# Performance work log

Hardware: AMD Instinct MI355X
Metric: run time of the kernel (lower is better)

Reference implementation:

```python
import jax, jax.numpy as jnp
import numpy as np

B, S, D = 8, 8192, 64   # D = 2**n_qubits, n_qubits = 6
D_MODEL = 1024
EPS = 1e-8


def setup_inputs() -> dict:
    key = jax.random.key(0)
    ks = jax.random.split(key, 7)
    return {
        "psi_Q": jax.random.normal(ks[0], (B, S, D), dtype=jnp.float32),
        "psi_K": jax.random.normal(ks[1], (B, S, D), dtype=jnp.float32),
        "psi_V": jax.random.normal(ks[2], (B, S, D), dtype=jnp.float32),
        "W1": jax.random.normal(ks[3], (1, D_MODEL), dtype=jnp.float32) * 0.02,
        "b1": jnp.zeros((D_MODEL,), dtype=jnp.float32),
        "W2": jax.random.normal(ks[4], (D_MODEL, D_MODEL), dtype=jnp.float32) * 0.02,
        "b2": jnp.zeros((D_MODEL,), dtype=jnp.float32),
    }


def _l2norm(x):
    return x / (jnp.linalg.norm(x, axis=-1, keepdims=True) + EPS)


def reference(psi_Q, psi_K, psi_V, W1, b1, W2, b2):
    # Normalize states (as the torch module does before StatePrep)
    q = _l2norm(psi_Q)
    k = _l2norm(psi_K)
    v = _l2norm(psi_V)
    state_dim = q.shape[-1]  # 2**n_qubits

    # attention_circuit probs[0]:
    # amplitude<0...0| = (H^{\otimes n} q)[0] * k[0] = sum(q)/sqrt(2^n) * k[0]
    att = (jnp.sum(q, axis=-1) ** 2) * (k[..., 0] ** 2) / state_dim  # [B,S]

    # value_circuit <Z_0>: wire 0 is MSB -> first half +1, second half -1
    half = state_dim // 2
    v2 = v * v
    v_exp = jnp.sum(v2[..., :half], axis=-1) - jnp.sum(v2[..., half:], axis=-1)  # [B,S]

    xi = (att * v_exp)[..., None]  # [B,S,1]

    h = jax.nn.relu(xi @ W1 + b1)   # [B,S,d_model]
    yQ = h @ W2 + b2                # [B,S,d_model]
    return yQ, xi
```

## Files before the change

### kernel.cpp

```cpp
#include <hip/hip_runtime.h>
#include <math.h>

#define BB 8
#define SS 8192
#define DD 64
#define DM 1024
#define EPSF 1e-8f
#define NROWS (BB * SS)
#define YQ_ELEMS ((size_t)NROWS * DM)

#define NPBLK 64

typedef float floatx4 __attribute__((ext_vector_type(4)));


__global__ __launch_bounds__(256) void qac_prep(
    const float* __restrict__ psiQ, const float* __restrict__ psiK,
    const float* __restrict__ psiV, const float* __restrict__ W1,
    const float* __restrict__ b1, const float* __restrict__ W2,
    const float* __restrict__ b2, float* __restrict__ ws,
    float* __restrict__ out) {
  const int t = threadIdx.x;

  if (blockIdx.x < NPBLK) {
    __shared__ float red[4][16][16];
    const int tn = t & 15;
    const int tm = t >> 4;
    const int nb = blockIdx.x;
    const int n = nb * 16 + tn;

    float up = 0.f, un = 0.f, dp = 0.f, dn = 0.f;
    const int m0 = tm * 64;
#pragma unroll 8
    for (int i = 0; i < 64; ++i) {
      const int m = m0 + i;
      const float w1 = W1[m];
      const float bv = b1[m];
      const float w2 = W2[(size_t)m * DM + n];
      const float wp = w1 > 0.f ? w1 : 0.f;
      const float wn = w1 < 0.f ? w1 : 0.f;
      const float bp = w1 > 0.f ? bv : 0.f;
      const float bn = w1 < 0.f ? bv : 0.f;
      up = fmaf(wp, w2, up);
      un = fmaf(wn, w2, un);
      dp = fmaf(bp, w2, dp);
      dn = fmaf(bn, w2, dn);
    }
    red[0][tm][tn] = up;
    red[1][tm][tn] = un;
    red[2][tm][tn] = dp;
    red[3][tm][tn] = dn;
    __syncthreads();
    if (t < 64) {
      const int q = t >> 4;
      const int col = t & 15;
      float s = 0.f;
#pragma unroll
      for (int j = 0; j < 16; ++j) s += red[q][j][col];
      const int n2 = nb * 16 + col;
      if (q < 2) {
        ws[q * DM + n2] = s;
      } else {
        ws[q * DM + n2] = b2[n2] + s;
      }
    }
    return;
  }

  const int g = t & 15;
  const int grp = t >> 4;
  const int row = (blockIdx.x - NPBLK) * 16 + grp;

  const float4 q = ((const float4*)(psiQ + (size_t)row * DD))[g];
  const float4 k = ((const float4*)(psiK + (size_t)row * DD))[g];
  const float4 v = ((const float4*)(psiV + (size_t)row * DD))[g];

  float sq = q.x + q.y + q.z + q.w;
  float sq2 = q.x * q.x + q.y * q.y + q.z * q.z + q.w * q.w;
  float sk2 = k.x * k.x + k.y * k.y + k.z * k.z + k.w * k.w;
  const float v2 = v.x * v.x + v.y * v.y + v.z * v.z + v.w * v.w;
  float va = (g < 8) ? v2 : 0.f;
  float vb = (g < 8) ? 0.f : v2;
  const float k0 = k.x;

#pragma unroll
  for (int m = 1; m < 16; m <<= 1) {
    sq += __shfl_xor(sq, m);
    sq2 += __shfl_xor(sq2, m);
    sk2 += __shfl_xor(sk2, m);
    va += __shfl_xor(va, m);
    vb += __shfl_xor(vb, m);
  }
  if (g == 0) {
    const float nq = sqrtf(sq2) + EPSF;
    const float nk = sqrtf(sk2) + EPSF;
    const float nv = sqrtf(va + vb) + EPSF;
    const float sqn = sq / nq;
    const float k0n = k0 / nk;
    const float att = sqn * sqn * k0n * k0n * (1.0f / 64.0f);
    const float vexp = (va - vb) / (nv * nv);
    out[YQ_ELEMS + row] = att * vexp;
  }
}

__global__ __launch_bounds__(256) void qac_stream(
    const float* __restrict__ ws, float* __restrict__ out) {
  __shared__ float xis[64];
  const int t = threadIdx.x;
  const int r0 = blockIdx.x * 64;
  if (t < 64) xis[t] = out[YQ_ELEMS + r0 + t];

  const float4 up = ((const float4*)(ws))[t];
  const float4 un = ((const float4*)(ws + DM))[t];
  const float4 cp = ((const float4*)(ws + 2 * DM))[t];
  const float4 cn = ((const float4*)(ws + 3 * DM))[t];
  __syncthreads();

#pragma unroll 8
  for (int r = 0; r < 64; ++r) {
    const float xi = xis[r];
    const bool pos = xi > 0.f;
    floatx4 o;
    o.x = fmaf(xi, pos ? up.x : un.x, pos ? cp.x : cn.x);
    o.y = fmaf(xi, pos ? up.y : un.y, pos ? cp.y : cn.y);
    o.z = fmaf(xi, pos ? up.z : un.z, pos ? cp.z : cn.z);
    o.w = fmaf(xi, pos ? up.w : un.w, pos ? cp.w : cn.w);
    floatx4* dst = (floatx4*)(out + (size_t)(r0 + r) * DM) + t;
    __builtin_nontemporal_store(o, dst);
  }
}

extern "C" void kernel_launch(void* const* d_in, const int* in_sizes, int n_in,
                              void* d_out, int out_size, void* d_ws, size_t ws_size,
                              hipStream_t stream) {
  const float* psiQ = (const float*)d_in[0];
  const float* psiK = (const float*)d_in[1];
  const float* psiV = (const float*)d_in[2];
  const float* W1 = (const float*)d_in[3];
  const float* b1 = (const float*)d_in[4];
  const float* W2 = (const float*)d_in[5];
  const float* b2 = (const float*)d_in[6];
  float* out = (float*)d_out;
  float* ws = (float*)d_ws;

  qac_prep<<<NPBLK + NROWS / 16, 256, 0, stream>>>(psiQ, psiK, psiV, W1, b1,
                                                   W2, b2, ws, out);
  qac_stream<<<NROWS / 64, 256, 0, stream>>>(ws, out);
}
```

Before: 63.98 us.

## Fuse per-row xi computation into the output streaming kernel

Splits the W1/W2 precompute into its own small kernel and moves the per-row quantum-state reductions into the streaming kernel, so each block computes its 64 xi values in shared memory before writing the output rows. This removes the global write and re-read of xi between kernels, and the first kernel is now tiny, so most of the work sits in a single pass. Input loads now use nontemporal hints. The risk is that the fused kernel's longer prologue delays the start of its store stream and may reduce overlap.

Measured after the change: 66.90 us. 1.05x slower.

```diff
diff --git a/kernel.cpp b/kernel.cpp
--- a/kernel.cpp
+++ b/kernel.cpp
@@ -9,112 +9,112 @@
 #define NROWS (BB * SS)
 #define YQ_ELEMS ((size_t)NROWS * DM)
 
-#define NPBLK 64
-
 typedef float floatx4 __attribute__((ext_vector_type(4)));
 
 
-__global__ __launch_bounds__(256) void qac_prep(
-    const float* __restrict__ psiQ, const float* __restrict__ psiK,
-    const float* __restrict__ psiV, const float* __restrict__ W1,
-    const float* __restrict__ b1, const float* __restrict__ W2,
-    const float* __restrict__ b2, float* __restrict__ ws,
-    float* __restrict__ out) {
+__global__ __launch_bounds__(256) void qac_part(
+    const float* __restrict__ W1, const float* __restrict__ b1,
+    const float* __restrict__ W2, const float* __restrict__ b2,
+    float* __restrict__ ws) {
+  __shared__ float red[4][16][16];
   const int t = threadIdx.x;
+  const int tn = t & 15;
+  const int tm = t >> 4;
+  const int nb = blockIdx.x;
+  const int n = nb * 16 + tn;
 
-  if (blockIdx.x < NPBLK) {
-    __shared__ float red[4][16][16];
-    const int tn = t & 15;
-    const int tm = t >> 4;
-    const int nb = blockIdx.x;
-    const int n = nb * 16 + tn;
-
-    float up = 0.f, un = 0.f, dp = 0.f, dn = 0.f;
-    const int m0 = tm * 64;
+  float up = 0.f, un = 0.f, dp = 0.f, dn = 0.f;
+  const int m0 = tm * 64;
 #pragma unroll 8
-    for (int i = 0; i < 64; ++i) {
-      const int m = m0 + i;
-      const float w1 = W1[m];
-      const float bv = b1[m];
-      const float w2 = W2[(size_t)m * DM + n];
-      const float wp = w1 > 0.f ? w1 : 0.f;
-      const float wn = w1 < 0.f ? w1 : 0.f;
-      const float bp = w1 > 0.f ? bv : 0.f;
-      const float bn = w1 < 0.f ? bv : 0.f;
-      up = fmaf(wp, w2, up);
-      un = fmaf(wn, w2, un);
-      dp = fmaf(bp, w2, dp);
-      dn = fmaf(bn, w2, dn);
+  for (int i = 0; i < 64; ++i) {
+    const int m = m0 + i;
+    const float w1 = W1[m];
+    const float bv = b1[m];
+    const float w2 = W2[(size_t)m * DM + n];
+    const float wp = w1 > 0.f ? w1 : 0.f;
+    const float wn = w1 < 0.f ? w1 : 0.f;
+    const float bp = w1 > 0.f ? bv : 0.f;
+    const float bn = w1 < 0.f ? bv : 0.f;
+    up = fmaf(wp, w2, up);
+    un = fmaf(wn, w2, un);
+    dp = fmaf(bp, w2, dp);
+    dn = fmaf(bn, w2, dn);
+  }
+  red[0][tm][tn] = up;
+  red[1][tm][tn] = un;
+  red[2][tm][tn] = dp;
+  red[3][tm][tn] = dn;
+  __syncthreads();
+  if (t < 64) {
+    const int q = t >> 4;
+    const int col = t & 15;
+    float s = 0.f;
+#pragma unroll
+    for (int j = 0; j < 16; ++j) s += red[q][j][col];
+    const int n2 = nb * 16 + col;
+    if (q < 2) {
+      ws[q * DM + n2] = s;
+    } else {
+      ws[q * DM + n2] = b2[n2] + s;
     }
-    red[0][tm][tn] = up;
-    red[1][tm][tn] = un;
-    red[2][tm][tn] = dp;
-    red[3][tm][tn] = dn;
-    __syncthreads();
-    if (t < 64) {
-      const int q = t >> 4;
-      const int col = t & 15;
-      float s = 0.f;
-#pragma unroll
-      for (int j = 0; j < 16; ++j) s += red[q][j][col];
-      const int n2 = nb * 16 + col;
-      if (q < 2) {
-        ws[q * DM + n2] = s;
-      } else {
-        ws[q * DM + n2] = b2[n2] + s;
-      }
-    }
-    return;
-  }
-
-  const int g = t & 15;
-  const int grp = t >> 4;
-  const int row = (blockIdx.x - NPBLK) * 16 + grp;
-
-  const float4 q = ((const float4*)(psiQ + (size_t)row * DD))[g];
-  const float4 k = ((const float4*)(psiK + (size_t)row * DD))[g];
-  const float4 v = ((const float4*)(psiV + (size_t)row * DD))[g];
-
-  float sq = q.x + q.y + q.z + q.w;
-  float sq2 = q.x * q.x + q.y * q.y + q.z * q.z + q.w * q.w;
-  float sk2 = k.x * k.x + k.y * k.y + k.z * k.z + k.w * k.w;
-  const float v2 = v.x * v.x + v.y * v.y + v.z * v.z + v.w * v.w;
-  float va = (g < 8) ? v2 : 0.f;
-  float vb = (g < 8) ? 0.f : v2;
-  const float k0 = k.x;
-
-#pragma unroll
-  for (int m = 1; m < 16; m <<= 1) {
-    sq += __shfl_xor(sq, m);
-    sq2 += __shfl_xor(sq2, m);
-    sk2 += __shfl_xor(sk2, m);
-    va += __shfl_xor(va, m);
-    vb += __shfl_xor(vb, m);
-  }
-  if (g == 0) {
-    const float nq = sqrtf(sq2) + EPSF;
-    const float nk = sqrtf(sk2) + EPSF;
-    const float nv = sqrtf(va + vb) + EPSF;
-    const float sqn = sq / nq;
-    const float k0n = k0 / nk;
-    const float att = sqn * sqn * k0n * k0n * (1.0f / 64.0f);
-    const float vexp = (va - vb) / (nv * nv);
-    out[YQ_ELEMS + row] = att * vexp;
   }
 }
 
-__global__ __launch_bounds__(256) void qac_stream(
-    const float* __restrict__ ws, float* __restrict__ out) {
+__global__ __launch_bounds__(256) void qac_fused(
+    const float* __restrict__ psiQ, const float* __restrict__ psiK,
+    const float* __restrict__ psiV, const float* __restrict__ ws,
+    float* __restrict__ out) {
   __shared__ float xis[64];
   const int t = threadIdx.x;
   const int r0 = blockIdx.x * 64;
-  if (t < 64) xis[t] = out[YQ_ELEMS + r0 + t];
+  const int g = t & 15;
+  const int grp = t >> 4;
 
   const float4 up = ((const float4*)(ws))[t];
   const float4 un = ((const float4*)(ws + DM))[t];
   const float4 cp = ((const float4*)(ws + 2 * DM))[t];
   const float4 cn = ((const float4*)(ws + 3 * DM))[t];
+
+#pragma unroll
+  for (int pass = 0; pass < 4; ++pass) {
+    const int row = r0 + pass * 16 + grp;
+    const floatx4 q = __builtin_nontemporal_load(
+        (const floatx4*)(psiQ + (size_t)row * DD) + g);
+    const floatx4 k = __builtin_nontemporal_load(
+        (const floatx4*)(psiK + (size_t)row * DD) + g);
+    const floatx4 v = __builtin_nontemporal_load(
+        (const floatx4*)(psiV + (size_t)row * DD) + g);
+
+    float sq = q.x + q.y + q.z + q.w;
+    float sq2 = q.x * q.x + q.y * q.y + q.z * q.z + q.w * q.w;
+    float sk2 = k.x * k.x + k.y * k.y + k.z * k.z + k.w * k.w;
+    const float v2 = v.x * v.x + v.y * v.y + v.z * v.z + v.w * v.w;
+    float va = (g < 8) ? v2 : 0.f;
+    float vb = (g < 8) ? 0.f : v2;
+    const float k0 = k.x;
+
+#pragma unroll
+    for (int m = 1; m < 16; m <<= 1) {
+      sq += __shfl_xor(sq, m);
+      sq2 += __shfl_xor(sq2, m);
+      sk2 += __shfl_xor(sk2, m);
+      va += __shfl_xor(va, m);
+      vb += __shfl_xor(vb, m);
+    }
+    if (g == 0) {
+      const float nq = sqrtf(sq2) + EPSF;
+      const float nk = sqrtf(sk2) + EPSF;
+      const float nv = sqrtf(va + vb) + EPSF;
+      const float sqn = sq / nq;
+      const float k0n = k0 / nk;
+      const float att = sqn * sqn * k0n * k0n * (1.0f / 64.0f);
+      const float vexp = (va - vb) / (nv * nv);
+      xis[pass * 16 + grp] = att * vexp;
+    }
+  }
   __syncthreads();
+
+  if (t < 64) out[YQ_ELEMS + r0 + t] = xis[t];
 
 #pragma unroll 8
   for (int r = 0; r < 64; ++r) {
@@ -143,7 +143,6 @@
   float* out = (float*)d_out;
   float* ws = (float*)d_ws;
 
-  qac_prep<<<NPBLK + NROWS / 16, 256, 0, stream>>>(psiQ, psiK, psiV, W1, b1,
-                                                   W2, b2, ws, out);
-  qac_stream<<<NROWS / 64, 256, 0, stream>>>(ws, out);
+  qac_part<<<64, 256, 0, stream>>>(W1, b1, W2, b2, ws);
+  qac_fused<<<NROWS / 64, 256, 0, stream>>>(psiQ, psiK, psiV, ws, out);
 }
```
